# Optimization experiments

Measured on AMD Instinct MI355X. Metric: run time of the kernel, lower is better.

The kernel has to match this reference:

```python
import jax, jax.numpy as jnp
import numpy as np
from jax import lax

D_MODEL = 384
D_INNER = 768          # expand * d_model
D_HALF = D_INNER // 2  # 384
D_STATE = 16
D_CONV = 4
DT_RANK = 24           # ceil(384/16)
BATCH = 8
SEQLEN = 4097
EXTRAS = 1
LMAIN = SEQLEN - EXTRAS


def setup_inputs() -> dict:
    key = jax.random.key(0)
    ks = jax.random.split(key, 12)
    hidden_states = jax.random.normal(ks[0], (BATCH, SEQLEN, D_MODEL), jnp.float32)
    in_proj_w = jax.random.normal(ks[1], (D_INNER, D_MODEL), jnp.float32) * 0.02
    conv_x_w = jax.random.normal(ks[2], (D_HALF, 1, D_CONV), jnp.float32) * 0.2
    conv_z_w = jax.random.normal(ks[3], (D_HALF, 1, D_CONV), jnp.float32) * 0.2
    x_proj_w = jax.random.normal(ks[4], (DT_RANK + 2 * D_STATE, D_HALF), jnp.float32) * 0.02
    dt_std = DT_RANK ** -0.5
    dt_proj_w = jax.random.uniform(ks[5], (D_HALF, DT_RANK), jnp.float32, -dt_std, dt_std)
    # bias = inverse softplus of dt sampled log-uniform in [1e-3, 1e-1]
    dt = jnp.exp(jax.random.uniform(ks[6], (D_HALF,), jnp.float32)
                 * (jnp.log(0.1) - jnp.log(0.001)) + jnp.log(0.001))
    dt = jnp.clip(dt, 1e-4, None)
    dt_proj_b = dt + jnp.log(-jnp.expm1(-dt))
    A_log = jnp.log(jnp.broadcast_to(jnp.arange(1, D_STATE + 1, dtype=jnp.float32),
                                     (D_HALF, D_STATE)))
    D_param = jnp.ones((D_HALF,), jnp.float32)
    out_proj_w = jax.random.normal(ks[7], (D_MODEL, D_HALF), jnp.float32) * 0.02
    perm = jax.random.permutation(ks[8], LMAIN).astype(jnp.int64)
    perm_rev = jnp.argsort(perm).astype(jnp.int64)
    return {
        "hidden_states": hidden_states,
        "in_proj_w": in_proj_w,
        "conv_x_w": conv_x_w,
        "conv_z_w": conv_z_w,
        "x_proj_w": x_proj_w,
        "dt_proj_w": dt_proj_w,
        "dt_proj_b": dt_proj_b,
        "A_log": A_log,
        "D_param": D_param,
        "out_proj_w": out_proj_w,
        "perm": perm,
        "perm_rev": perm_rev,
    }


def _depthwise_conv_same(x, w):
    # x: (B, C, L), w: (C, 1, K); torch padding='same' for k=4 -> pad (left=1, right=2)
    total = D_CONV - 1
    left = total // 2
    return lax.conv_general_dilated(
        x, w, window_strides=(1,), padding=[(left, total - left)],
        dimension_numbers=("NCH", "OIH", "NCH"), feature_group_count=D_HALF)


def _selective_scan(x, dt, A, Bm, Cm, D_param, delta_bias):
    # x, dt: (B, d, L); A: (d, n); Bm, Cm: (B, n, L)
    dt = jax.nn.softplus(dt + delta_bias[None, :, None])
    xT = jnp.moveaxis(x, 2, 0)    # (L, B, d)
    dtT = jnp.moveaxis(dt, 2, 0)  # (L, B, d)
    BT = jnp.moveaxis(Bm, 2, 0)   # (L, B, n)
    CT = jnp.moveaxis(Cm, 2, 0)   # (L, B, n)

    def step(h, inp):
        x_t, dt_t, B_t, C_t = inp
        dA = jnp.exp(dt_t[..., None] * A)                      # (B, d, n)
        h = h * dA + (dt_t * x_t)[..., None] * B_t[:, None, :]  # (B, d, n)
        y = jnp.einsum("bdn,bn->bd", h, C_t)
        return h, y

    h0 = jnp.zeros((x.shape[0], x.shape[1], A.shape[1]), x.dtype)
    _, ys = lax.scan(step, h0, (xT, dtT, BT, CT))
    y = jnp.moveaxis(ys, 0, 2)  # (B, d, L)
    return y + D_param[None, :, None] * x


def reference(hidden_states, in_proj_w, conv_x_w, conv_z_w, x_proj_w,
              dt_proj_w, dt_proj_b, A_log, D_param, out_proj_w, perm, perm_rev):
    # in_proj (no bias): (B,L,D) -> (B, d_inner, L)
    xz = jnp.einsum("bld,ed->bel", hidden_states, in_proj_w)
    # hilbert/zigzag reorder on the main (non-extra) tokens
    xz = jnp.concatenate([xz[:, :, :EXTRAS], xz[:, :, EXTRAS:][:, :, perm]], axis=2)

    x, z = jnp.split(xz, 2, axis=1)  # (B, d_half, L) each
    A = -jnp.exp(A_log)
    x = jax.nn.silu(_depthwise_conv_same(x, conv_x_w))
    z = jax.nn.silu(_depthwise_conv_same(z, conv_z_w))

    x_dbl = jnp.einsum("bdl,ed->bel", x, x_proj_w)  # (B, dt_rank+2n, L)
    dt_low, Bm, Cm = jnp.split(x_dbl, [DT_RANK, DT_RANK + D_STATE], axis=1)
    dt = jnp.einsum("brl,dr->bdl", dt_low, dt_proj_w)

    y = _selective_scan(x, dt, A, Bm, Cm, D_param, dt_proj_b)
    y = (y * z).transpose(0, 2, 1)  # (B, L, d_half)
    out = jnp.einsum("bld,ed->ble", y, out_proj_w)  # (B, L, D)
    # undo the permutation on the output
    out = jnp.concatenate([out[:, :EXTRAS], out[:, EXTRAS:][:, perm_rev]], axis=1)
    return out
```

## Files before the change

### kernel.cpp

```cpp
#include <hip/hip_runtime.h>
#include <hip/hip_bf16.h>

#define DEVI __device__ __forceinline__

constexpr int B_   = 8;
constexpr int L_   = 4097;
constexpr int MTOT = B_ * L_;
constexpr int DH   = 384;
constexpr int NS   = 16;
constexpr int CH   = 33;
constexpr int NCH  = (L_ + CH - 1) / CH;

typedef __bf16 bf16x8 __attribute__((ext_vector_type(8)));
typedef float  f32x4  __attribute__((ext_vector_type(4)));

DEVI float bl(unsigned v) { return __uint_as_float(v << 16); }
DEVI float bh(unsigned v) { return __uint_as_float(v & 0xffff0000u); }
DEVI float bf(const __hip_bfloat16 x) { return __bfloat162float(x); }
DEVI unsigned short f2bu(float x) {
  __hip_bfloat16 b = __float2bfloat16(x);
  return *(unsigned short*)&b;
}
DEVI float u16f(const uint4& u, int j) {
  const unsigned w = (&u.x)[j >> 1];
  return (j & 1) ? bh(w) : bl(w);
}
DEVI float softplus_f(float x) {
  return (x > 20.f) ? x : __logf(1.f + __expf(x));
}

DEVI void gld16(const __hip_bfloat16* g, __hip_bfloat16* l) {
  __builtin_amdgcn_global_load_lds(
      (const __attribute__((address_space(1))) void*)g,
      (__attribute__((address_space(3))) void*)l, 16, 0, 0);
}

__global__ void flag_k(const void* hs, int* flagp) {
  if (threadIdx.x == 0 && blockIdx.x == 0) {
    const unsigned short* u = (const unsigned short*)hs;
    int ok = 1;
    for (int i = 0; i < 8; ++i) {
      const unsigned short v = u[2 * i];
      const int e = (v >> 7) & 0xFF;
      if (!(v == 0 || (e >= 100 && e <= 140))) ok = 0;
    }
    flagp[0] = ok;
    flagp[1] = 1;
  }
}

__global__ void a2prep_k(const void* __restrict__ alog, float* __restrict__ a2fo,
                         int* flagp) {
  const int d = threadIdx.x;
  const int f = flagp[0];
  float a2[16];
#pragma unroll
  for (int n = 0; n < 16; ++n) {
    const float v = f ? bf(((const __hip_bfloat16*)alog)[d * 16 + n])
                      : ((const float*)alog)[d * 16 + n];
    a2[n] = -1.4426950408889634f * __expf(v);
    a2fo[d * 16 + n] = a2[n];
  }
  int ok = 1;
#pragma unroll
  for (int n = 1; n < 16; ++n) {
    const float ref = (float)(n + 1) * a2[0];
    if (fabsf(a2[n] - ref) > 1e-3f * fabsf(ref)) ok = 0;
  }
  if (!ok) atomicAnd(&flagp[1], 0);
}

__global__ void perm_k(const int* p0, const int* p1, int* d0, int* d1) {
  __shared__ int s_or;
  const int* src = blockIdx.x ? p1 : p0;
  int*       dst = blockIdx.x ? d1 : d0;
  if (threadIdx.x == 0) s_or = 0;
  __syncthreads();
  int loc = 0;
  for (int i = threadIdx.x; i < 2048; i += 1024) loc |= src[2 * i + 1];
  atomicOr(&s_or, loc);
  __syncthreads();
  const bool is64 = (s_or == 0);
  for (int j = threadIdx.x; j < 4096; j += 1024)
    dst[j] = is64 ? (int)((const long long*)src)[j] : src[j];
}

struct NormSet { const void* src[8]; void* dst[8]; int n[8]; };
__global__ void norm_all(NormSet s, const int* flagp) {
  const int idx = blockIdx.x * 256 + threadIdx.x;
  const int f = flagp[0];
#pragma unroll
  for (int t = 0; t < 8; ++t) {
    if (idx < s.n[t]) {
      __hip_bfloat16* d = (__hip_bfloat16*)s.dst[t];
      if (f) d[idx] = ((const __hip_bfloat16*)s.src[t])[idx];
      else   d[idx] = __float2bfloat16(((const float*)s.src[t])[idx]);
    }
  }
}

__global__ void prep_k(const __hip_bfloat16* __restrict__ dtw,
                       const __hip_bfloat16* __restrict__ xw,
                       __hip_bfloat16* __restrict__ wcomb) {
  const int idx = blockIdx.x * 256 + threadIdx.x;
  if (idx >= 512 * 384) return;
  const int n = idx / 384, k = idx - n * 384;
  float v = 0.f;
  if (n < 384) {
#pragma unroll
    for (int r = 0; r < 24; ++r) v += bf(dtw[n * 24 + r]) * bf(xw[r * 384 + k]);
  } else if (n < 416) {
    v = bf(xw[(24 + n - 384) * 384 + k]);
  }
  wcomb[idx] = __float2bfloat16(v);
}

__global__ void cvt_k(const void* __restrict__ hs, __hip_bfloat16* __restrict__ dst,
                      const int* __restrict__ gidx, const int* __restrict__ flagp) {
  const int idx = blockIdx.x * 256 + threadIdx.x;
  if (idx >= MTOT * 48) return;
  const int j = idx % 48;
  const int r = idx / 48;
  const int b = r / L_, t = r - b * L_;
  const int src = b * L_ + (t == 0 ? 0 : 1 + gidx[t - 1]);
  uint4 o;
  if (flagp[0]) {
    o = *(const uint4*)((const __hip_bfloat16*)hs + (size_t)src * 384 + j * 8);
  } else {
    const float* f = (const float*)hs + (size_t)src * 384 + j * 8;
    const float4 f0 = *(const float4*)f;
    const float4 f1 = *(const float4*)(f + 4);
    o.x = f2bu(f0.x) | ((unsigned)f2bu(f0.y) << 16);
    o.y = f2bu(f0.z) | ((unsigned)f2bu(f0.w) << 16);
    o.z = f2bu(f1.x) | ((unsigned)f2bu(f1.y) << 16);
    o.w = f2bu(f1.z) | ((unsigned)f2bu(f1.w) << 16);
  }
  *(uint4*)(dst + (size_t)r * 384 + j * 8) = o;
}

template<int GATHER, int EPI>
__global__ __launch_bounds__(256, 3)
void gemm_k(const __hip_bfloat16* __restrict__ A, const __hip_bfloat16* __restrict__ W,
            void* __restrict__ e0, void* __restrict__ e1,
            const __hip_bfloat16* __restrict__ bias,
            const int* __restrict__ gidx, const int* __restrict__ flagp,
            int M, int N)
{
  __shared__ __align__(16) char smem[36864];
  __hip_bfloat16* lA = (__hip_bfloat16*)smem;
  __hip_bfloat16* lB = lA + 2 * 128 * 32;
  const int tid  = threadIdx.x;
  const int lane = tid & 63;
  const int wv   = tid >> 6;
  const int wm   = wv >> 1, wn = wv & 1;
  const int lrow = lane & 15, quad = lane >> 4;
  const int fbf  = flagp[0];

  const int NT = gridDim.x;
  const int nblocks = NT * (int)gridDim.y;
  const int id = blockIdx.y * NT + blockIdx.x;
  const int q8 = nblocks >> 3, r8 = nblocks & 7;
  const int xcd = id & 7, slot = id >> 3;
  const int nid = (xcd < r8 ? xcd * (q8 + 1)
                            : r8 * (q8 + 1) + (xcd - r8) * q8) + slot;
  const int mt = nid / NT, nt = nid - mt * NT;

  const bool live = !(EPI == 1 && nt * 128 + wn * 64 >= 416);

  const __hip_bfloat16* aSrc[4];
  const __hip_bfloat16* bSrc[4];
  __hip_bfloat16* aDst[4];
  __hip_bfloat16* bDst[4];
#pragma unroll
  for (int p = 0; p < 4; ++p) {
    const int s   = p * 256 + tid;
    const int kh  = s >> 9;
    const int row = (s >> 2) & 127;
    const int kc  = kh * 32 + (s & 3) * 8;
    int r = mt * 128 + row;
    if (r >= M) r = M - 1;
    int src;
    if (GATHER) { const int b = r / L_, t = r - b * L_;
                  src = b * L_ + (t == 0 ? 0 : 1 + gidx[t - 1]); }
    else        { src = r; }
    aSrc[p] = A + (size_t)src * 384 + kc;
    bSrc[p] = W + (size_t)(nt * 128 + row) * 384 + kc;
    aDst[p] = &lA[s * 8];
    bDst[p] = &lB[s * 8];
  }

  f32x4 acc[4][4] = {};

#pragma unroll
  for (int kt = 0; kt < 6; ++kt) {
    __syncthreads();
#pragma unroll
    for (int p = 0; p < 4; ++p) gld16(aSrc[p] + kt * 64, aDst[p]);
#pragma unroll
    for (int p = 0; p < 4; ++p) gld16(bSrc[p] + kt * 64, bDst[p]);
    __syncthreads();
    if (live) {
#pragma unroll
      for (int kh = 0; kh < 2; ++kh) {
        bf16x8 af[4], bfr[4];
#pragma unroll
        for (int i = 0; i < 4; ++i)
          af[i] = *reinterpret_cast<const bf16x8*>(
              &lA[kh * 4096 + (wm * 64 + i * 16 + lrow) * 32 + quad * 8]);
#pragma unroll
        for (int j = 0; j < 4; ++j)
          bfr[j] = *reinterpret_cast<const bf16x8*>(
              &lB[kh * 4096 + (wn * 64 + j * 16 + lrow) * 32 + quad * 8]);
#pragma unroll
        for (int i = 0; i < 4; ++i)
#pragma unroll
          for (int j = 0; j < 4; ++j)
            acc[i][j] = __builtin_amdgcn_mfma_f32_16x16x32_bf16(af[i], bfr[j], acc[i][j], 0, 0, 0);
      }
    }
  }

  const int r0c = mt * 128;
  if (EPI == 1 && nt == 3) {
#pragma unroll
    for (int i = 0; i < 4; ++i) {
      const int row0 = r0c + wm * 64 + i * 16 + quad * 4;
#pragma unroll
      for (int j = 0; j < 4; ++j) {
        const int col = 384 + wn * 64 + j * 16 + lrow;
        if (col >= 416) continue;
#pragma unroll
        for (int rg = 0; rg < 4; ++rg) {
          const int r = row0 + rg;
          if (r >= M) continue;
          ((float*)e1)[(size_t)r * 32 + (col - 384)] = acc[i][j][rg];
        }
      }
    }
  } else if (EPI == 2 && !fbf) {
    float* lT = (float*)smem;
#pragma unroll
    for (int h = 0; h < 2; ++h) {
      __syncthreads();
      if (wn == h) {
#pragma unroll
        for (int i = 0; i < 4; ++i)
#pragma unroll
          for (int j = 0; j < 4; ++j)
#pragma unroll
            for (int rg = 0; rg < 4; ++rg)
              lT[(wm * 64 + i * 16 + quad * 4 + rg) * 72 + j * 16 + lrow] = acc[i][j][rg];
      }
      __syncthreads();
#pragma unroll
      for (int p = 0; p < 8; ++p) {
        const int ch = p * 256 + tid;
        const int row = ch >> 4, c4 = (ch & 15) * 4;
        const int r = r0c + row;
        if (r < M) {
          const float4 v = *(const float4*)&lT[row * 72 + c4];
          *(float4*)((float*)e0 + (size_t)r * 384 + nt * 128 + h * 64 + c4) = v;
        }
      }
    }
  } else {
    __hip_bfloat16* lT = (__hip_bfloat16*)smem;
#pragma unroll
    for (int h = 0; h < 2; ++h) {
      __syncthreads();
      if (wn == h) {
        float bj[4] = {};
        if (EPI == 1) {
#pragma unroll
          for (int j = 0; j < 4; ++j)
            bj[j] = bf(bias[nt * 128 + h * 64 + j * 16 + lrow]);
        }
#pragma unroll
        for (int i = 0; i < 4; ++i)
#pragma unroll
          for (int j = 0; j < 4; ++j)
#pragma unroll
            for (int rg = 0; rg < 4; ++rg) {
              float v = acc[i][j][rg];
              if (EPI == 1) v = softplus_f(v + bj[j]);
              lT[(wm * 64 + i * 16 + quad * 4 + rg) * 72 + j * 16 + lrow] =
                  __float2bfloat16(v);
            }
      }
      __syncthreads();
#pragma unroll
      for (int p = 0; p < 4; ++p) {
        const int ch = p * 256 + tid;
        const int row = ch >> 3, c8 = (ch & 7) * 8;
        const int r = r0c + row;
        if (r < M) {
          const uint4 v = *(const uint4*)&lT[row * 72 + c8];
          const int g = nt * 128 + h * 64 + c8;
          __hip_bfloat16* dst = (EPI == 0 && g >= 384)
                ? (__hip_bfloat16*)e1 + (size_t)r * 384 + (g - 384)
                : (__hip_bfloat16*)e0 + (size_t)r * 384 + g;
          *(uint4*)dst = v;
        }
      }
    }
  }
}

__global__ void convx_k(const __hip_bfloat16* __restrict__ xh,
                        const __hip_bfloat16* __restrict__ cxw,
                        __hip_bfloat16* __restrict__ xc) {
  const int idx = blockIdx.x * 256 + threadIdx.x;
  if (idx >= MTOT * 48) return;
  const int g  = idx % 48;
  const int rg = idx / 48;
  const int t  = rg % L_;
  const int c0 = g * 8;
  uint4 wv[4];
#pragma unroll
  for (int p = 0; p < 4; ++p) wv[p] = *(const uint4*)(cxw + c0 * 4 + p * 8);
  float acc[8] = {};
#pragma unroll
  for (int k = 0; k < 4; ++k) {
    const int tt = t + k - 1;
    if (tt < 0 || tt >= L_) continue;
    const uint4 u = *(const uint4*)(xh + (size_t)(rg + k - 1) * 384 + c0);
#pragma unroll
    for (int j = 0; j < 8; ++j) {
      const int e = j * 4 + k;
      acc[j] += u16f(wv[e >> 3], e & 7) * u16f(u, j);
    }
  }
  uint4 o;
#pragma unroll
  for (int p = 0; p < 4; ++p) {
    const float s0 = acc[2 * p]     / (1.f + __expf(-acc[2 * p]));
    const float s1 = acc[2 * p + 1] / (1.f + __expf(-acc[2 * p + 1]));
    (&o.x)[p] = f2bu(s0) | ((unsigned)f2bu(s1) << 16);
  }
  *(uint4*)(xc + (size_t)rg * 384 + c0) = o;
}

__global__ __launch_bounds__(128)
void scan1_k(const __hip_bfloat16* __restrict__ dt, const float* __restrict__ bc,
             __hip_bfloat16* xcio,
             const float* __restrict__ a2f,
             const __hip_bfloat16* __restrict__ dpar,
             float* __restrict__ pbuf, float* __restrict__ hend,
             const int* __restrict__ flagp)
{
  __shared__ __align__(16) float lBC[CH * 32];
  const int blk = blockIdx.x;
  const int dt3 = blk % 3;
  const int c   = (blk / 3) % NCH;
  const int b   = blk / (3 * NCH);
  const int d   = dt3 * 128 + threadIdx.x;
  const int t0  = c * CH;
  const int r0  = b * L_ + t0;
  const int tmax = (L_ - t0 < CH) ? (L_ - t0) : CH;
  for (int i = threadIdx.x; i < tmax * 32; i += 128) lBC[i] = bc[(size_t)r0 * 32 + i];
  __syncthreads();

  float h[16];
#pragma unroll
  for (int n = 0; n < 16; ++n) h[n] = 0.f;
  float sdt = 0.f;
  const float Dd = bf(dpar[d]);
  const size_t base = ((size_t)(c * 8 + b) * 16) * 384 + d;

  float dtv = bf(dt[(size_t)r0 * 384 + d]);
  float xv  = bf(xcio[(size_t)r0 * 384 + d]);

  if (flagp[1]) {
    const float a2b = a2f[d * 16];
    for (int tt = 0; tt < tmax; ++tt) {
      const size_t r = (size_t)(r0 + tt);
      float dtv_n = 0.f, xv_n = 0.f;
      if (tt + 1 < tmax) {
        dtv_n = bf(dt[(r + 1) * 384 + d]);
        xv_n  = bf(xcio[(r + 1) * 384 + d]);
      }
      sdt += dtv;
      const float dtx = dtv * xv;
      float pw[17];
      pw[1] = exp2f(dtv * a2b);
#pragma unroll
      for (int n = 2; n <= 16; ++n) pw[n] = pw[n >> 1] * pw[n - (n >> 1)];
      float4 bq[4], cq[4];
#pragma unroll
      for (int q = 0; q < 4; ++q) {
        bq[q] = *(const float4*)&lBC[tt * 32 + q * 4];
        cq[q] = *(const float4*)&lBC[tt * 32 + 16 + q * 4];
      }
      float ya = 0.f, yb = 0.f;
#pragma unroll
      for (int n = 0; n < 16; ++n) {
        h[n] = h[n] * pw[n + 1] + dtx * (&bq[n >> 2].x)[n & 3];
        const float t = h[n] * (&cq[n >> 2].x)[n & 3];
        if (n & 1) yb += t; else ya += t;
      }
      const float y = ya + yb + Dd * xv;
      xcio[r * 384 + d] = __float2bfloat16(y);
      dtv = dtv_n; xv = xv_n;
    }
    float Ep[17];
    Ep[1] = exp2f(sdt * a2b);
#pragma unroll
    for (int n = 2; n <= 16; ++n) Ep[n] = Ep[n >> 1] * Ep[n - (n >> 1)];
#pragma unroll
    for (int n = 0; n < 16; ++n) {
      pbuf[base + n * 384] = Ep[n + 1];
      hend[base + n * 384] = h[n];
    }
  } else {
    float a2[16];
#pragma unroll
    for (int n = 0; n < 16; ++n) a2[n] = a2f[d * 16 + n];
    for (int tt = 0; tt < tmax; ++tt) {
      const size_t r = (size_t)(r0 + tt);
      float dtv_n = 0.f, xv_n = 0.f;
      if (tt + 1 < tmax) {
        dtv_n = bf(dt[(r + 1) * 384 + d]);
        xv_n  = bf(xcio[(r + 1) * 384 + d]);
      }
      sdt += dtv;
      const float dtx = dtv * xv;
      float4 bq[4], cq[4];
#pragma unroll
      for (int q = 0; q < 4; ++q) {
        bq[q] = *(const float4*)&lBC[tt * 32 + q * 4];
        cq[q] = *(const float4*)&lBC[tt * 32 + 16 + q * 4];
      }
      float ya = 0.f, yb = 0.f;
#pragma unroll
      for (int n = 0; n < 16; ++n) {
        h[n] = h[n] * exp2f(dtv * a2[n]) + dtx * (&bq[n >> 2].x)[n & 3];
        const float t = h[n] * (&cq[n >> 2].x)[n & 3];
        if (n & 1) yb += t; else ya += t;
      }
      const float y = ya + yb + Dd * xv;
      xcio[r * 384 + d] = __float2bfloat16(y);
      dtv = dtv_n; xv = xv_n;
    }
#pragma unroll
    for (int n = 0; n < 16; ++n) {
      pbuf[base + n * 384] = exp2f(sdt * a2[n]);
      hend[base + n * 384] = h[n];
    }
  }
}

__global__ void scan2_k(float* __restrict__ pbuf, const float* __restrict__ hend) {
  const int tid = blockIdx.x * 256 + threadIdx.x;
  const int d = tid % 384;
  const int n = (tid / 384) & 15;
  const int b = tid / 6144;
  float H = 0.f;
  for (int c = 0; c < NCH; ++c) {
    const size_t idx = ((size_t)(c * 8 + b) * 16 + n) * 384 + d;
    const float p = pbuf[idx];
    const float he = hend[idx];
    pbuf[idx] = H;
    H = p * H + he;
  }
}

__global__ __launch_bounds__(128)
void scan3_k(__hip_bfloat16* dtyg, const float* __restrict__ bc,
             const __hip_bfloat16* __restrict__ yl,
             const __hip_bfloat16* __restrict__ zh,
             const __hip_bfloat16* __restrict__ czw,
             const float* __restrict__ a2f,
             const float* __restrict__ hstart,
             const int* __restrict__ flagp)
{
  __shared__ __align__(16) float lC[CH * 16];
  const int blk = blockIdx.x;
  const int dt3 = blk % 3;
  const int c   = (blk / 3) % NCH;
  const int b   = blk / (3 * NCH);
  const int d   = dt3 * 128 + threadIdx.x;
  const int t0  = c * CH;
  const int r0  = b * L_ + t0;
  const int tmax = (L_ - t0 < CH) ? (L_ - t0) : CH;
  for (int i = threadIdx.x; i < tmax * 16; i += 128)
    lC[i] = bc[(size_t)r0 * 32 + (i >> 4) * 32 + 16 + (i & 15)];
  __syncthreads();

  float hs_[16];
  const size_t base = ((size_t)(c * 8 + b) * 16) * 384 + d;
#pragma unroll
  for (int n = 0; n < 16; ++n) hs_[n] = hstart[base + n * 384];
  float cw[4];
#pragma unroll
  for (int k = 0; k < 4; ++k) cw[k] = bf(czw[d * 4 + k]);

  float zm1 = (t0 - 1 >= 0) ? bf(zh[(size_t)(r0 - 1) * 384 + d]) : 0.f;
  float z0  = bf(zh[(size_t)r0 * 384 + d]);
  float zp1 = (t0 + 1 < L_) ? bf(zh[(size_t)(r0 + 1) * 384 + d]) : 0.f;
  float sdt = 0.f;

  float dtv = bf(dtyg[(size_t)r0 * 384 + d]);
  float ylv = bf(yl[(size_t)r0 * 384 + d]);

  if (flagp[1]) {
    const float a2b = a2f[d * 16];
    for (int tt = 0; tt < tmax; ++tt) {
      const int t = t0 + tt;
      const size_t r = (size_t)(r0 + tt);
      const float zp2 = (t + 2 < L_) ? bf(zh[(r + 2) * 384 + d]) : 0.f;
      float dtv_n = 0.f, ylv_n = 0.f;
      if (tt + 1 < tmax) {
        dtv_n = bf(dtyg[(r + 1) * 384 + d]);
        ylv_n = bf(yl[(r + 1) * 384 + d]);
      }
      sdt += dtv;
      float pw[17];
      pw[1] = exp2f(sdt * a2b);
#pragma unroll
      for (int n = 2; n <= 16; ++n) pw[n] = pw[n >> 1] * pw[n - (n >> 1)];
      float4 cq[4];
#pragma unroll
      for (int q = 0; q < 4; ++q) cq[q] = *(const float4*)&lC[tt * 16 + q * 4];
      float ca = 0.f, cb = 0.f;
#pragma unroll
      for (int n = 0; n < 16; ++n) {
        const float t2 = (&cq[n >> 2].x)[n & 3] * hs_[n] * pw[n + 1];
        if (n & 1) cb += t2; else ca += t2;
      }
      const float y = ylv + ca + cb;
      const float zc = cw[0] * zm1 + cw[1] * z0 + cw[2] * zp1 + cw[3] * zp2;
      const float zs = zc / (1.f + __expf(-zc));
      dtyg[r * 384 + d] = __float2bfloat16(y * zs);
      zm1 = z0; z0 = zp1; zp1 = zp2;
      dtv = dtv_n; ylv = ylv_n;
    }
  } else {
    float a2[16];
#pragma unroll
    for (int n = 0; n < 16; ++n) a2[n] = a2f[d * 16 + n];
    for (int tt = 0; tt < tmax; ++tt) {
      const int t = t0 + tt;
      const size_t r = (size_t)(r0 + tt);
      const float zp2 = (t + 2 < L_) ? bf(zh[(r + 2) * 384 + d]) : 0.f;
      float dtv_n = 0.f, ylv_n = 0.f;
      if (tt + 1 < tmax) {
        dtv_n = bf(dtyg[(r + 1) * 384 + d]);
        ylv_n = bf(yl[(r + 1) * 384 + d]);
      }
      sdt += dtv;
      float4 cq[4];
#pragma unroll
      for (int q = 0; q < 4; ++q) cq[q] = *(const float4*)&lC[tt * 16 + q * 4];
      float ca = 0.f, cb = 0.f;
#pragma unroll
      for (int n = 0; n < 16; ++n) {
        const float t2 = (&cq[n >> 2].x)[n & 3] * hs_[n] * exp2f(sdt * a2[n]);
        if (n & 1) cb += t2; else ca += t2;
      }
      const float y = ylv + ca + cb;
      const float zc = cw[0] * zm1 + cw[1] * z0 + cw[2] * zp1 + cw[3] * zp2;
      const float zs = zc / (1.f + __expf(-zc));
      dtyg[r * 384 + d] = __float2bfloat16(y * zs);
      zm1 = z0; z0 = zp1; zp1 = zp2;
      dtv = dtv_n; ylv = ylv_n;
    }
  }
}

extern "C" void kernel_launch(void* const* d_in, const int* in_sizes, int n_in,
                              void* d_out, int out_size, void* d_ws, size_t ws_size,
                              hipStream_t stream) {
  const void* hs   = d_in[0];
  const void* w_in = d_in[1];
  const void* cxw  = d_in[2];
  const void* czw  = d_in[3];
  const void* xw   = d_in[4];
  const void* dtw  = d_in[5];
  const void* dtb  = d_in[6];
  const void* alog = d_in[7];
  const void* dpar = d_in[8];
  const void* ow   = d_in[9];
  const int* perm  = (const int*)d_in[10];
  const int* permr = (const int*)d_in[11];

  char* ws = (char*)d_ws;
  size_t off = 0;
  auto alloc = [&](size_t nbytes) -> char* {
    char* p = ws + off;
    off += (nbytes + 255) & ~(size_t)255;
    return p;
  };
  int* flag              = (int*)alloc(256);
  int* nperm             = (int*)alloc(4096 * 4);
  int* npermr            = (int*)alloc(4096 * 4);
  float* a2f             = (float*)alloc(6144 * 4);
  __hip_bfloat16* w_inb  = (__hip_bfloat16*)alloc(294912 * 2);
  __hip_bfloat16* cxwb   = (__hip_bfloat16*)alloc(1536 * 2);
  __hip_bfloat16* czwb   = (__hip_bfloat16*)alloc(1536 * 2);
  __hip_bfloat16* xwb    = (__hip_bfloat16*)alloc(21504 * 2);
  __hip_bfloat16* dtwb   = (__hip_bfloat16*)alloc(9216 * 2);
  __hip_bfloat16* dtbb   = (__hip_bfloat16*)alloc(384 * 2);
  __hip_bfloat16* dparb  = (__hip_bfloat16*)alloc(384 * 2);
  __hip_bfloat16* owb    = (__hip_bfloat16*)alloc(147456 * 2);
  __hip_bfloat16* wcombb = (__hip_bfloat16*)alloc((size_t)512 * 384 * 2);
  __hip_bfloat16* hsb    = (__hip_bfloat16*)alloc((size_t)MTOT * 384 * 2);
  __hip_bfloat16* zh     = (__hip_bfloat16*)alloc((size_t)MTOT * 384 * 2);
  __hip_bfloat16* xc     = (__hip_bfloat16*)alloc((size_t)MTOT * 384 * 2);
  __hip_bfloat16* dtyg   = (__hip_bfloat16*)alloc((size_t)MTOT * 384 * 2);
  float*          bcf    = (float*)alloc((size_t)MTOT * 32 * 4);
  __hip_bfloat16* xh   = (__hip_bfloat16*)d_out;
  float*          pbuf = (float*)d_out;
  float*          hend = (float*)((char*)d_out + (size_t)NCH * B_ * NS * DH * 4);

  flag_k<<<1, 64, 0, stream>>>(hs, flag);
  perm_k<<<2, 1024, 0, stream>>>(perm, permr, nperm, npermr);
  a2prep_k<<<1, 384, 0, stream>>>(alog, a2f, flag);
  NormSet ns;
  ns.src[0] = w_in; ns.dst[0] = w_inb; ns.n[0] = 294912;
  ns.src[1] = ow;   ns.dst[1] = owb;   ns.n[1] = 147456;
  ns.src[2] = xw;   ns.dst[2] = xwb;   ns.n[2] = 21504;
  ns.src[3] = dtw;  ns.dst[3] = dtwb;  ns.n[3] = 9216;
  ns.src[4] = cxw;  ns.dst[4] = cxwb;  ns.n[4] = 1536;
  ns.src[5] = czw;  ns.dst[5] = czwb;  ns.n[5] = 1536;
  ns.src[6] = dtb;  ns.dst[6] = dtbb;  ns.n[6] = 384;
  ns.src[7] = dpar; ns.dst[7] = dparb; ns.n[7] = 384;
  norm_all<<<1152, 256, 0, stream>>>(ns, flag);
  prep_k<<<768, 256, 0, stream>>>(dtwb, xwb, wcombb);
  cvt_k<<<(MTOT * 48 + 255) / 256, 256, 0, stream>>>(hs, hsb, nperm, flag);
  gemm_k<0, 0><<<dim3(6, 257), 256, 0, stream>>>(
      hsb, w_inb, xh, zh, nullptr, nullptr, flag, MTOT, 768);
  convx_k<<<(MTOT * 48 + 255) / 256, 256, 0, stream>>>(xh, cxwb, xc);
  gemm_k<0, 1><<<dim3(4, 257), 256, 0, stream>>>(
      xc, wcombb, dtyg, bcf, dtbb, nullptr, flag, MTOT, 512);
  scan1_k<<<B_ * NCH * 3, 128, 0, stream>>>(dtyg, bcf, xc, a2f, dparb, pbuf, hend, flag);
  scan2_k<<<192, 256, 0, stream>>>(pbuf, hend);
  scan3_k<<<B_ * NCH * 3, 128, 0, stream>>>(dtyg, bcf, xc, zh, czwb, a2f, pbuf, flag);
  gemm_k<1, 2><<<dim3(3, 257), 256, 0, stream>>>(
      dtyg, owb, d_out, nullptr, nullptr, npermr, flag, MTOT, 384);
  (void)in_sizes; (void)n_in; (void)out_size; (void)ws_size;
}
```

Baseline: 332.3 us.

## Merge small setup kernels, raise GEMM occupancy bound, add restrict to scan pointers

Folds the flag-detection and permutation-conversion kernels into one launch, and moves the A_log preprocessing into an extra block of the weight-normalization kernel. Together this removes two kernel launches and their per-launch overhead. It also raises the GEMM launch bound from 3 to 4 waves per SIMD, which caps register use so more blocks can be resident, at the risk of spilling. Finally it marks two scan kernel pointers __restrict__ so the compiler has more freedom to schedule loads.

```diff
diff --git a/kernel.cpp b/kernel.cpp
--- a/kernel.cpp
+++ b/kernel.cpp
@@ -35,45 +35,25 @@
       (__attribute__((address_space(3))) void*)l, 16, 0, 0);
 }
 
-__global__ void flag_k(const void* hs, int* flagp) {
-  if (threadIdx.x == 0 && blockIdx.x == 0) {
-    const unsigned short* u = (const unsigned short*)hs;
-    int ok = 1;
-    for (int i = 0; i < 8; ++i) {
-      const unsigned short v = u[2 * i];
-      const int e = (v >> 7) & 0xFF;
-      if (!(v == 0 || (e >= 100 && e <= 140))) ok = 0;
-    }
-    flagp[0] = ok;
-    flagp[1] = 1;
-  }
-}
-
-__global__ void a2prep_k(const void* __restrict__ alog, float* __restrict__ a2fo,
-                         int* flagp) {
-  const int d = threadIdx.x;
-  const int f = flagp[0];
-  float a2[16];
-#pragma unroll
-  for (int n = 0; n < 16; ++n) {
-    const float v = f ? bf(((const __hip_bfloat16*)alog)[d * 16 + n])
-                      : ((const float*)alog)[d * 16 + n];
-    a2[n] = -1.4426950408889634f * __expf(v);
-    a2fo[d * 16 + n] = a2[n];
-  }
-  int ok = 1;
-#pragma unroll
-  for (int n = 1; n < 16; ++n) {
-    const float ref = (float)(n + 1) * a2[0];
-    if (fabsf(a2[n] - ref) > 1e-3f * fabsf(ref)) ok = 0;
-  }
-  if (!ok) atomicAnd(&flagp[1], 0);
-}
-
-__global__ void perm_k(const int* p0, const int* p1, int* d0, int* d1) {
+__global__ void init_k(const void* hs, int* flagp,
+                       const int* p0, const int* p1, int* d0, int* d1) {
+  if (blockIdx.x == 0) {
+    if (threadIdx.x == 0) {
+      const unsigned short* u = (const unsigned short*)hs;
+      int ok = 1;
+      for (int i = 0; i < 8; ++i) {
+        const unsigned short v = u[2 * i];
+        const int e = (v >> 7) & 0xFF;
+        if (!(v == 0 || (e >= 100 && e <= 140))) ok = 0;
+      }
+      flagp[0] = ok;
+      flagp[1] = 1;
+    }
+    return;
+  }
   __shared__ int s_or;
-  const int* src = blockIdx.x ? p1 : p0;
-  int*       dst = blockIdx.x ? d1 : d0;
+  const int* src = (blockIdx.x == 2) ? p1 : p0;
+  int*       dst = (blockIdx.x == 2) ? d1 : d0;
   if (threadIdx.x == 0) s_or = 0;
   __syncthreads();
   int loc = 0;
@@ -86,9 +66,30 @@
 }
 
 struct NormSet { const void* src[8]; void* dst[8]; int n[8]; };
-__global__ void norm_all(NormSet s, const int* flagp) {
+__global__ void norm_all(NormSet s, int* flagp,
+                         const void* __restrict__ alog, float* __restrict__ a2fo) {
+  const int f = flagp[0];
+  if (blockIdx.x == 1152) {
+    int ok = 1;
+    for (int d = threadIdx.x; d < 384; d += 256) {
+      float a2[16];
+#pragma unroll
+      for (int n = 0; n < 16; ++n) {
+        const float v = f ? bf(((const __hip_bfloat16*)alog)[d * 16 + n])
+                          : ((const float*)alog)[d * 16 + n];
+        a2[n] = -1.4426950408889634f * __expf(v);
+        a2fo[d * 16 + n] = a2[n];
+      }
+#pragma unroll
+      for (int n = 1; n < 16; ++n) {
+        const float ref = (float)(n + 1) * a2[0];
+        if (fabsf(a2[n] - ref) > 1e-3f * fabsf(ref)) ok = 0;
+      }
+    }
+    if (!ok) atomicAnd(&flagp[1], 0);
+    return;
+  }
   const int idx = blockIdx.x * 256 + threadIdx.x;
-  const int f = flagp[0];
 #pragma unroll
   for (int t = 0; t < 8; ++t) {
     if (idx < s.n[t]) {
@@ -139,7 +140,7 @@
 }
 
 template<int GATHER, int EPI>
-__global__ __launch_bounds__(256, 3)
+__global__ __launch_bounds__(256, 4)
 void gemm_k(const __hip_bfloat16* __restrict__ A, const __hip_bfloat16* __restrict__ W,
             void* __restrict__ e0, void* __restrict__ e1,
             const __hip_bfloat16* __restrict__ bias,
@@ -342,7 +343,7 @@
 
 __global__ __launch_bounds__(128)
 void scan1_k(const __hip_bfloat16* __restrict__ dt, const float* __restrict__ bc,
-             __hip_bfloat16* xcio,
+             __hip_bfloat16* __restrict__ xcio,
              const float* __restrict__ a2f,
              const __hip_bfloat16* __restrict__ dpar,
              float* __restrict__ pbuf, float* __restrict__ hend,
@@ -465,7 +466,7 @@
 }
 
 __global__ __launch_bounds__(128)
-void scan3_k(__hip_bfloat16* dtyg, const float* __restrict__ bc,
+void scan3_k(__hip_bfloat16* __restrict__ dtyg, const float* __restrict__ bc,
              const __hip_bfloat16* __restrict__ yl,
              const __hip_bfloat16* __restrict__ zh,
              const __hip_bfloat16* __restrict__ czw,
@@ -612,9 +613,7 @@
   float*          pbuf = (float*)d_out;
   float*          hend = (float*)((char*)d_out + (size_t)NCH * B_ * NS * DH * 4);
 
-  flag_k<<<1, 64, 0, stream>>>(hs, flag);
-  perm_k<<<2, 1024, 0, stream>>>(perm, permr, nperm, npermr);
-  a2prep_k<<<1, 384, 0, stream>>>(alog, a2f, flag);
+  init_k<<<3, 1024, 0, stream>>>(hs, flag, perm, permr, nperm, npermr);
   NormSet ns;
   ns.src[0] = w_in; ns.dst[0] = w_inb; ns.n[0] = 294912;
   ns.src[1] = ow;   ns.dst[1] = owb;   ns.n[1] = 147456;
@@ -624,7 +623,7 @@
   ns.src[5] = czw;  ns.dst[5] = czwb;  ns.n[5] = 1536;
   ns.src[6] = dtb;  ns.dst[6] = dtbb;  ns.n[6] = 384;
   ns.src[7] = dpar; ns.dst[7] = dparb; ns.n[7] = 384;
-  norm_all<<<1152, 256, 0, stream>>>(ns, flag);
+  norm_all<<<1153, 256, 0, stream>>>(ns, flag, alog, a2f);
   prep_k<<<768, 256, 0, stream>>>(dtwb, xwb, wcombb);
   cvt_k<<<(MTOT * 48 + 255) / 256, 256, 0, stream>>>(hs, hsb, nperm, flag);
   gemm_k<0, 0><<<dim3(6, 257), 256, 0, stream>>>(
```

New measurement: 334.1 us. About the same (+0.5%).
